# Optimization experiments

Hardware: AMD Instinct MI355X
Metric: run time of the kernel (lower is better)

Reference implementation:

```python
import jax, jax.numpy as jnp
import numpy as np

SM_SCALE = 0.08838834764831845  # 1/sqrt(128)
SLIDING_WINDOW = 128
N_TOKENS, N_HEADS, Q_MULT, D_HEAD = 2048, 8, 4, 128


def setup_inputs() -> dict:
    key = jax.random.key(0)
    k1, k2, k3, k4 = jax.random.split(key, 4)
    Q = jax.random.normal(k1, (N_TOKENS, N_HEADS, Q_MULT, D_HEAD), dtype=jnp.float32)
    K = jax.random.normal(k2, (N_TOKENS, N_HEADS, D_HEAD), dtype=jnp.float32)
    V = jax.random.normal(k3, (N_TOKENS, N_HEADS, D_HEAD), dtype=jnp.float32)
    S = jax.random.normal(k4, (N_HEADS * Q_MULT,), dtype=jnp.float32)
    return {"Q": Q, "K": K, "V": V, "S": S}


def _build_mask(n_tokens, sliding_window, dtype):
    q_idx = jnp.arange(n_tokens)[:, None]
    k_idx = jnp.arange(n_tokens)[None, :]
    # causal: disallow k > q; sliding window: disallow k <= q - sliding_window
    disallowed = k_idx > q_idx
    if sliding_window > 0:
        disallowed = disallowed | (k_idx <= q_idx - sliding_window)
    return jnp.where(disallowed, jnp.array(-jnp.inf, dtype), jnp.array(0.0, dtype))


def reference(Q, K, V, S):
    n_tokens, n_heads, q_mult, d_head = Q.shape
    mask = _build_mask(n_tokens, SLIDING_WINDOW, Q.dtype)  # (T, T)
    # scores: (h, m, q, k)
    QK = jnp.einsum('qhmd,khd->hmqk', Q, K) * SM_SCALE
    QK = QK + mask[None, None, :, :]
    # append per-(head, q_mult) sink logit as an extra key column
    sink = jnp.broadcast_to(S.reshape(n_heads, q_mult, 1, 1),
                            (n_heads, q_mult, n_tokens, 1))
    QK = jnp.concatenate([QK, sink], axis=-1)  # (h, m, q, k+1)
    W = jax.nn.softmax(QK, axis=-1)[..., :-1]  # drop sink column
    attn = jnp.einsum('hmqk,khd->qhmd', W, V)
    return attn.reshape(n_tokens, n_heads * q_mult * d_head)
```

## Files before the change

kernel.cpp:

```cpp
#include <hip/hip_runtime.h>
#include <cstdint>

#define T_TOK 2048
#define NH 8
#define QM 4
#define DH 128
#define BQ 16
#define ROWS 64
#define CK 32
#define MAXCH 5
#define KS 136
#define VS 40
#define PS 40
#define SM_SCALE 0.08838834764831845f

typedef __attribute__((ext_vector_type(8))) short short8v;
typedef __attribute__((ext_vector_type(4))) short short4v;
typedef __attribute__((ext_vector_type(4))) float floatx4;

static __device__ __forceinline__ short f2bf(float x) {
  union { float f; unsigned u; } v; v.f = x;
  unsigned r = (v.u + 0x7fffu + ((v.u >> 16) & 1u)) >> 16;
  return (short)r;
}

__global__ __launch_bounds__(256, 4)
void attn_fwd(const float* __restrict__ Qp, const float* __restrict__ Kp,
              const float* __restrict__ Vp, const float* __restrict__ Sp,
              float* __restrict__ Op) {
  __shared__ short k_s[CK * KS];
  __shared__ short v_s[DH * VS];
  __shared__ short p_s[ROWS * PS];

  const int t    = threadIdx.x;
  const int lane = t & 63;
  const int wave = t >> 6;
  const int quad = lane >> 4;
  const int l16  = lane & 15;

  const int bx = blockIdx.x;
  const int h  = bx & 7;
  const int q0 = (bx >> 3) * BQ;
  const int lo0  = q0 > 127 ? q0 - 127 : 0;
  const int qmax = q0 + BQ - 1;
  const int nk   = qmax - lo0 + 1;

  const int Ra = wave * 16 + l16;
  const int qa = q0 + (Ra >> 2), ma = Ra & 3;
  const float* qptr = Qp + ((size_t)qa * (NH * QM) + h * QM + ma) * DH + quad * 8;
  short8v qf[4];
#pragma unroll
  for (int s = 0; s < 4; ++s) {
    float4 x0 = *(const float4*)(qptr + 32 * s);
    float4 x1 = *(const float4*)(qptr + 32 * s + 4);
    short8v f;
    f[0] = f2bf(x0.x); f[1] = f2bf(x0.y); f[2] = f2bf(x0.z); f[3] = f2bf(x0.w);
    f[4] = f2bf(x1.x); f[5] = f2bf(x1.y); f[6] = f2bf(x1.z); f[7] = f2bf(x1.w);
    qf[s] = f;
  }

  const int qc = q0 + wave * 4 + quad;
  float mx[4], dn[4];
#pragma unroll
  for (int r = 0; r < 4; ++r) { mx[r] = Sp[h * QM + r]; dn[r] = 1.0f; }

  floatx4 oacc[8];
#pragma unroll
  for (int nt = 0; nt < 8; ++nt) oacc[nt] = (floatx4)0.0f;

  for (int c = 0; c < MAXCH; ++c) {
    const int kb = lo0 + c * CK;
    if (c * CK >= nk) break;
    __syncthreads();

    {
      const int jj = t >> 5, d4 = (t & 31) * 4;
#pragma unroll
      for (int pass = 0; pass < 4; ++pass) {
        int j = jj + pass * 8;
        int g = kb + j; g = g < T_TOK ? g : T_TOK - 1;
        float4 kv = *(const float4*)(Kp + ((size_t)g * NH + h) * DH + d4);
        short4v pk;
        pk[0] = f2bf(kv.x); pk[1] = f2bf(kv.y); pk[2] = f2bf(kv.z); pk[3] = f2bf(kv.w);
        *(short4v*)(k_s + j * KS + d4) = pk;
      }
    }
    {
      const int d = t & 127;
      const int g0 = t >> 7;
#pragma unroll
      for (int rep = 0; rep < 2; ++rep) {
        int grp = g0 + rep * 2;
        short8v pv;
#pragma unroll
        for (int j = 0; j < 8; ++j) {
          int g = kb + grp * 8 + j; g = g < T_TOK ? g : T_TOK - 1;
          pv[j] = f2bf(Vp[((size_t)g * NH + h) * DH + d]);
        }
        *(short8v*)(v_s + d * VS + grp * 8) = pv;
      }
    }
    __syncthreads();

    floatx4 sc0 = (floatx4)0.0f, sc1 = (floatx4)0.0f;
#pragma unroll
    for (int s = 0; s < 4; ++s) {
      short8v k0 = *(const short8v*)(k_s + l16 * KS + quad * 8 + 32 * s);
      short8v k1 = *(const short8v*)(k_s + (l16 + 16) * KS + quad * 8 + 32 * s);
      sc0 = __builtin_amdgcn_mfma_f32_16x16x32_bf16(qf[s], k0, sc0, 0, 0, 0);
      sc1 = __builtin_amdgcn_mfma_f32_16x16x32_bf16(qf[s], k1, sc1, 0, 0, 0);
    }

    const int k0i = kb + l16, k1i = kb + 16 + l16;
    const bool ok0 = (k0i <= qc) && (k0i > qc - 128);
    const bool ok1 = (k1i <= qc) && (k1i > qc - 128);
    float al[4];
#pragma unroll
    for (int r = 0; r < 4; ++r) {
      float s0 = ok0 ? sc0[r] * SM_SCALE : -1e30f;
      float s1 = ok1 ? sc1[r] * SM_SCALE : -1e30f;
      float cm = fmaxf(s0, s1);
#pragma unroll
      for (int mm = 1; mm <= 8; mm <<= 1) cm = fmaxf(cm, __shfl_xor(cm, mm));
      float mxn = fmaxf(mx[r], cm);
      al[r] = __expf(mx[r] - mxn);
      float e0 = __expf(s0 - mxn);
      float e1 = __expf(s1 - mxn);
      float ps = e0 + e1;
#pragma unroll
      for (int mm = 1; mm <= 8; mm <<= 1) ps += __shfl_xor(ps, mm);
      dn[r] = dn[r] * al[r] + ps;
      mx[r] = mxn;
      const int R = wave * 16 + quad * 4 + r;
      p_s[R * PS + l16]      = f2bf(e0);
      p_s[R * PS + 16 + l16] = f2bf(e1);
    }

#pragma unroll
    for (int nt = 0; nt < 8; ++nt)
#pragma unroll
      for (int r = 0; r < 4; ++r) oacc[nt][r] *= al[r];

    short8v pf = *(const short8v*)(p_s + (wave * 16 + l16) * PS + quad * 8);
#pragma unroll
    for (int nt = 0; nt < 8; ++nt) {
      short8v vf = *(const short8v*)(v_s + (l16 + 16 * nt) * VS + quad * 8);
      oacc[nt] = __builtin_amdgcn_mfma_f32_16x16x32_bf16(pf, vf, oacc[nt], 0, 0, 0);
    }
  }

#pragma unroll
  for (int r = 0; r < 4; ++r) {
    float rd = 1.0f / dn[r];
    float* ob = Op + (size_t)qc * (NH * QM * DH) + ((size_t)h * QM + r) * DH + l16;
#pragma unroll
    for (int nt = 0; nt < 8; ++nt) ob[nt * 16] = oacc[nt][r] * rd;
  }
}

extern "C" void kernel_launch(void* const* d_in, const int* in_sizes, int n_in,
                              void* d_out, int out_size, void* d_ws, size_t ws_size,
                              hipStream_t stream) {
  const float* Q = (const float*)d_in[0];
  const float* K = (const float*)d_in[1];
  const float* V = (const float*)d_in[2];
  const float* S = (const float*)d_in[3];
  float* O = (float*)d_out;
  const int grid = (T_TOK / BQ) * NH;
  attn_fwd<<<dim3(grid), dim3(256), 0, stream>>>(Q, K, V, S, O);
}
```

Measured before the change: 111.6 us.

## Double-buffer K/V tiles, enlarge query block, and drop online-max softmax

Measured after the change: 104.4 us. 1.07x faster.

```diff
diff --git a/kernel.cpp b/kernel.cpp
--- a/kernel.cpp
+++ b/kernel.cpp
@@ -5,10 +5,9 @@
 #define NH 8
 #define QM 4
 #define DH 128
-#define BQ 16
-#define ROWS 64
+#define BQ 32
+#define ROWS 128
 #define CK 32
-#define MAXCH 5
 #define KS 136
 #define VS 40
 #define PS 40
@@ -20,32 +19,31 @@
 
 static __device__ __forceinline__ short f2bf(float x) {
   union { float f; unsigned u; } v; v.f = x;
-  unsigned r = (v.u + 0x7fffu + ((v.u >> 16) & 1u)) >> 16;
-  return (short)r;
+  return (short)((v.u + 0x7fffu + ((v.u >> 16) & 1u)) >> 16);
 }
 
-__global__ __launch_bounds__(256, 4)
+__global__ __launch_bounds__(512, 4)
 void attn_fwd(const float* __restrict__ Qp, const float* __restrict__ Kp,
               const float* __restrict__ Vp, const float* __restrict__ Sp,
               float* __restrict__ Op) {
-  __shared__ short k_s[CK * KS];
-  __shared__ short v_s[DH * VS];
+  __shared__ short k_s[2][CK * KS];
+  __shared__ short v_s[2][DH * VS];
   __shared__ short p_s[ROWS * PS];
 
   const int t    = threadIdx.x;
   const int lane = t & 63;
-  const int wave = t >> 6;
+  const int wv   = t >> 6;
   const int quad = lane >> 4;
   const int l16  = lane & 15;
 
   const int bx = blockIdx.x;
   const int h  = bx & 7;
   const int q0 = (bx >> 3) * BQ;
-  const int lo0  = q0 > 127 ? q0 - 127 : 0;
-  const int qmax = q0 + BQ - 1;
-  const int nk   = qmax - lo0 + 1;
+  const int lo0 = q0 > 127 ? q0 - 127 : 0;
+  const int nk  = q0 + BQ - lo0;
+  const int nch = (nk + CK - 1) >> 5;
 
-  const int Ra = wave * 16 + l16;
+  const int Ra = wv * 16 + l16;
   const int qa = q0 + (Ra >> 2), ma = Ra & 3;
   const float* qptr = Qp + ((size_t)qa * (NH * QM) + h * QM + ma) * DH + quad * 8;
   short8v qf[4];
@@ -59,54 +57,71 @@
     qf[s] = f;
   }
 
-  const int qc = q0 + wave * 4 + quad;
-  float mx[4], dn[4];
-#pragma unroll
-  for (int r = 0; r < 4; ++r) { mx[r] = Sp[h * QM + r]; dn[r] = 1.0f; }
+  const int kj  = t >> 5;
+  const int kd4 = (t & 31) * 4;
+  const int vd  = t & 127;
+  const int vg  = t >> 7;
 
+  const int qc = q0 + wv * 4 + quad;
+  float dn[4] = {0.f, 0.f, 0.f, 0.f};
   floatx4 oacc[8];
 #pragma unroll
   for (int nt = 0; nt < 8; ++nt) oacc[nt] = (floatx4)0.0f;
 
-  for (int c = 0; c < MAXCH; ++c) {
+  float4 pk[2];
+  float  pv[8];
+  {
+    const int kb = lo0;
+#pragma unroll
+    for (int p = 0; p < 2; ++p) {
+      int g = kb + kj + 16 * p; g = g < T_TOK ? g : T_TOK - 1;
+      pk[p] = *(const float4*)(Kp + ((size_t)g * NH + h) * DH + kd4);
+    }
+#pragma unroll
+    for (int j = 0; j < 8; ++j) {
+      int g = kb + vg * 8 + j; g = g < T_TOK ? g : T_TOK - 1;
+      pv[j] = Vp[((size_t)g * NH + h) * DH + vd];
+    }
+  }
+
+  for (int c = 0; c < nch; ++c) {
+    const int b  = c & 1;
     const int kb = lo0 + c * CK;
-    if (c * CK >= nk) break;
+
+#pragma unroll
+    for (int p = 0; p < 2; ++p) {
+      short4v s4;
+      s4[0] = f2bf(pk[p].x); s4[1] = f2bf(pk[p].y);
+      s4[2] = f2bf(pk[p].z); s4[3] = f2bf(pk[p].w);
+      *(short4v*)(&k_s[b][(kj + 16 * p) * KS + kd4]) = s4;
+    }
+    {
+      short8v s8;
+#pragma unroll
+      for (int j = 0; j < 8; ++j) s8[j] = f2bf(pv[j]);
+      *(short8v*)(&v_s[b][vd * VS + vg * 8]) = s8;
+    }
     __syncthreads();
 
-    {
-      const int jj = t >> 5, d4 = (t & 31) * 4;
+    if (c + 1 < nch) {
+      const int kb2 = kb + CK;
 #pragma unroll
-      for (int pass = 0; pass < 4; ++pass) {
-        int j = jj + pass * 8;
-        int g = kb + j; g = g < T_TOK ? g : T_TOK - 1;
-        float4 kv = *(const float4*)(Kp + ((size_t)g * NH + h) * DH + d4);
-        short4v pk;
-        pk[0] = f2bf(kv.x); pk[1] = f2bf(kv.y); pk[2] = f2bf(kv.z); pk[3] = f2bf(kv.w);
-        *(short4v*)(k_s + j * KS + d4) = pk;
+      for (int p = 0; p < 2; ++p) {
+        int g = kb2 + kj + 16 * p; g = g < T_TOK ? g : T_TOK - 1;
+        pk[p] = *(const float4*)(Kp + ((size_t)g * NH + h) * DH + kd4);
+      }
+#pragma unroll
+      for (int j = 0; j < 8; ++j) {
+        int g = kb2 + vg * 8 + j; g = g < T_TOK ? g : T_TOK - 1;
+        pv[j] = Vp[((size_t)g * NH + h) * DH + vd];
       }
     }
-    {
-      const int d = t & 127;
-      const int g0 = t >> 7;
-#pragma unroll
-      for (int rep = 0; rep < 2; ++rep) {
-        int grp = g0 + rep * 2;
-        short8v pv;
-#pragma unroll
-        for (int j = 0; j < 8; ++j) {
-          int g = kb + grp * 8 + j; g = g < T_TOK ? g : T_TOK - 1;
-          pv[j] = f2bf(Vp[((size_t)g * NH + h) * DH + d]);
-        }
-        *(short8v*)(v_s + d * VS + grp * 8) = pv;
-      }
-    }
-    __syncthreads();
 
     floatx4 sc0 = (floatx4)0.0f, sc1 = (floatx4)0.0f;
 #pragma unroll
     for (int s = 0; s < 4; ++s) {
-      short8v k0 = *(const short8v*)(k_s + l16 * KS + quad * 8 + 32 * s);
-      short8v k1 = *(const short8v*)(k_s + (l16 + 16) * KS + quad * 8 + 32 * s);
+      short8v k0 = *(const short8v*)(&k_s[b][l16 * KS + quad * 8 + 32 * s]);
+      short8v k1 = *(const short8v*)(&k_s[b][(l16 + 16) * KS + quad * 8 + 32 * s]);
       sc0 = __builtin_amdgcn_mfma_f32_16x16x32_bf16(qf[s], k0, sc0, 0, 0, 0);
       sc1 = __builtin_amdgcn_mfma_f32_16x16x32_bf16(qf[s], k1, sc1, 0, 0, 0);
     }
@@ -114,44 +129,31 @@
     const int k0i = kb + l16, k1i = kb + 16 + l16;
     const bool ok0 = (k0i <= qc) && (k0i > qc - 128);
     const bool ok1 = (k1i <= qc) && (k1i > qc - 128);
-    float al[4];
 #pragma unroll
     for (int r = 0; r < 4; ++r) {
-      float s0 = ok0 ? sc0[r] * SM_SCALE : -1e30f;
-      float s1 = ok1 ? sc1[r] * SM_SCALE : -1e30f;
-      float cm = fmaxf(s0, s1);
-#pragma unroll
-      for (int mm = 1; mm <= 8; mm <<= 1) cm = fmaxf(cm, __shfl_xor(cm, mm));
-      float mxn = fmaxf(mx[r], cm);
-      al[r] = __expf(mx[r] - mxn);
-      float e0 = __expf(s0 - mxn);
-      float e1 = __expf(s1 - mxn);
-      float ps = e0 + e1;
-#pragma unroll
-      for (int mm = 1; mm <= 8; mm <<= 1) ps += __shfl_xor(ps, mm);
-      dn[r] = dn[r] * al[r] + ps;
-      mx[r] = mxn;
-      const int R = wave * 16 + quad * 4 + r;
+      float e0 = ok0 ? __expf(sc0[r] * SM_SCALE) : 0.f;
+      float e1 = ok1 ? __expf(sc1[r] * SM_SCALE) : 0.f;
+      dn[r] += e0 + e1;
+      const int R = wv * 16 + quad * 4 + r;
       p_s[R * PS + l16]      = f2bf(e0);
       p_s[R * PS + 16 + l16] = f2bf(e1);
     }
 
-#pragma unroll
-    for (int nt = 0; nt < 8; ++nt)
-#pragma unroll
-      for (int r = 0; r < 4; ++r) oacc[nt][r] *= al[r];
-
-    short8v pf = *(const short8v*)(p_s + (wave * 16 + l16) * PS + quad * 8);
+    short8v pf = *(const short8v*)(&p_s[(wv * 16 + l16) * PS + quad * 8]);
 #pragma unroll
     for (int nt = 0; nt < 8; ++nt) {
-      short8v vf = *(const short8v*)(v_s + (l16 + 16 * nt) * VS + quad * 8);
+      short8v vf = *(const short8v*)(&v_s[b][(l16 + 16 * nt) * VS + quad * 8]);
       oacc[nt] = __builtin_amdgcn_mfma_f32_16x16x32_bf16(pf, vf, oacc[nt], 0, 0, 0);
     }
   }
 
 #pragma unroll
   for (int r = 0; r < 4; ++r) {
-    float rd = 1.0f / dn[r];
+    float s = dn[r];
+#pragma unroll
+    for (int mm = 1; mm <= 8; mm <<= 1) s += __shfl_xor(s, mm);
+    const float total = s + __expf(Sp[h * QM + r]);
+    const float rd = 1.0f / total;
     float* ob = Op + (size_t)qc * (NH * QM * DH) + ((size_t)h * QM + r) * DH + l16;
 #pragma unroll
     for (int nt = 0; nt < 8; ++nt) ob[nt * 16] = oacc[nt][r] * rd;
@@ -167,5 +169,5 @@
   const float* S = (const float*)d_in[3];
   float* O = (float*)d_out;
   const int grid = (T_TOK / BQ) * NH;
-  attn_fwd<<<dim3(grid), dim3(256), 0, stream>>>(Q, K, V, S, O);
+  attn_fwd<<<dim3(grid), dim3(512), 0, stream>>>(Q, K, V, S, O);
 }
```
